# Performance work log

Measured on AMD Instinct MI355X. Metric: run time of the kernel, lower is better.

Reference implementation:

```python
import jax, jax.numpy as jnp
import numpy as np

N = 2048        # num nodes
E = 65536       # num edges
C_IN = 128      # in_channels
C = 128         # out_channels (must equal C_IN for stacked layers)
H = 8           # heads
WALK_LEN = 4
NEG_SLOPE = 0.2


def compute_mask(edge_index, n, walk_length):
    # dense adjacency with duplicate-edge summation (matches sparse_coo to_dense) + self loops
    adj = jnp.zeros((n, n), jnp.float32).at[edge_index[0], edge_index[1]].add(1.0)
    adj = adj + jnp.eye(n, dtype=jnp.float32)
    kernel = jnp.eye(n, dtype=jnp.float32)
    result = kernel
    for _ in range(walk_length):
        kernel = kernel @ adj
        result = result + kernel
    # F.normalize(p=2, dim=1)
    norm = jnp.linalg.norm(result, axis=1, keepdims=True)
    return result / jnp.maximum(norm, 1e-12)


def gkat_layer(x, edge_index, mask, lin_w, att):
    n = x.shape[0]
    xh = (x @ lin_w.T).reshape(n, H, C)              # [N,H,C]
    src, dst = edge_index[0], edge_index[1]          # x_j = xh[src], x_i = xh[dst]
    att_i = att[0, :, :C]                            # [H,C]
    att_j = att[0, :, C:]                            # [H,C]
    # cat([x_i,x_j],-1)*att summed == x_i.att_i + x_j.att_j, computed per node then gathered
    s_i = jnp.einsum('nhc,hc->nh', xh, att_i)
    s_j = jnp.einsum('nhc,hc->nh', xh, att_j)
    alpha = s_i[dst] + s_j[src]                      # [E,H]
    alpha = jnp.where(alpha >= 0, alpha, NEG_SLOPE * alpha)
    alpha = alpha * mask[src, dst][:, None]          # graph-kernel mask per edge
    alpha = jax.nn.softmax(alpha, axis=0)            # global softmax over edges (faithful to F.softmax dim=0)
    # dropout: eval mode -> identity
    msg = xh[src] * alpha[:, :, None]                # [E,H,C]
    out = jax.ops.segment_sum(msg, dst, num_segments=n)  # scatter-add aggregate
    return out.mean(axis=1)                          # head mean -> [N,C]


def setup_inputs() -> dict:
    key = jax.random.key(0)
    ks = jax.random.split(key, 8)
    x = jax.random.normal(ks[0], (N, C_IN), jnp.float32)
    edge_index = jax.random.randint(ks[1], (2, E), 0, N, jnp.int64)
    # xavier-uniform-ish init
    def xav(k, shape):
        fan_in, fan_out = shape[-1], shape[0] if len(shape) == 2 else shape[-1]
        lim = float(np.sqrt(6.0 / (fan_in + fan_out)))
        return jax.random.uniform(k, shape, jnp.float32, -lim, lim)
    lin_w0 = xav(ks[2], (H * C, C_IN))
    att0 = xav(ks[3], (1, H, 2 * C))
    lin_w1 = xav(ks[4], (H * C, C))
    att1 = xav(ks[5], (1, H, 2 * C))
    skip_w = xav(ks[6], (C, C_IN))
    skip_b = jnp.zeros((C,), jnp.float32)
    return {"x": x, "edge_index": edge_index, "lin_w0": lin_w0, "att0": att0,
            "lin_w1": lin_w1, "att1": att1, "skip_w": skip_w, "skip_b": skip_b}


def reference(x, edge_index, lin_w0, att0, lin_w1, att1, skip_w, skip_b):
    mask = compute_mask(edge_index, x.shape[0], WALK_LEN)  # identical for both layers
    x_skip = x @ skip_w.T + skip_b
    h = jax.nn.relu(gkat_layer(x, edge_index, mask, lin_w0, att0))
    h = jax.nn.relu(gkat_layer(h, edge_index, mask, lin_w1, att1))
    return h + x_skip
```

## Files before the change

### kernel.cpp

```cpp
#include <hip/hip_runtime.h>
#include <hip/hip_bf16.h>

#define NN 2048
#define EE 65536
#define HH 8
#define CC 128
#define HC 1024
#define NEG_SLOPE 0.2f

__device__ __forceinline__ unsigned fenc(float f) {
    unsigned u = __float_as_uint(f);
    return (u & 0x80000000u) ? ~u : (u | 0x80000000u);
}
__device__ __forceinline__ float fdec(unsigned e) {
    return (e & 0x80000000u) ? __uint_as_float(e ^ 0x80000000u) : __uint_as_float(~e);
}

__global__ void k_deg(const int* __restrict__ ei, int* __restrict__ deg) {
    int e = blockIdx.x * 256 + threadIdx.x;
    atomicAdd(&deg[ei[EE + e]], 1);
}

__global__ void k_scan(const int* __restrict__ deg, int* __restrict__ offs) {
    __shared__ int buf[2][NN];
    int t = threadIdx.x;
    for (int i = t; i < NN; i += 1024) buf[0][i] = deg[i];
    __syncthreads();
    int cur = 0;
    for (int off = 1; off < NN; off <<= 1) {
        for (int i = t; i < NN; i += 1024) {
            int v = buf[cur][i];
            if (i >= off) v += buf[cur][i - off];
            buf[cur ^ 1][i] = v;
        }
        __syncthreads();
        cur ^= 1;
    }
    if (t == 0) offs[0] = 0;
    for (int i = t; i < NN; i += 1024) offs[i + 1] = buf[cur][i];
}

__global__ void k_scatter(const int* __restrict__ ei, const int* __restrict__ offs,
                          int* __restrict__ cursor, int* __restrict__ elist) {
    int e = blockIdx.x * 256 + threadIdx.x;
    int d = ei[EE + e];
    int p = atomicAdd(&cursor[d], 1);
    elist[offs[d] + p] = e;
}

__global__ __launch_bounds__(256) void k_build_M(
    const int* __restrict__ offs, const int* __restrict__ elist,
    const int* __restrict__ ei, unsigned short* __restrict__ M) {
    int d = blockIdx.x, t = threadIdx.x;
    __shared__ float col[NN];
    __shared__ int s_b[256], s_l[256];
    for (int i = t; i < NN; i += 256) col[i] = 0.f;
    int beg = offs[d], end = offs[d + 1];
    for (int base = beg; base < end; base += 256) {
        int m = min(256, end - base);
        __syncthreads();
        if (t < m) {
            int s = ei[elist[base + t]];
            int b = offs[s];
            s_b[t] = b;
            s_l[t] = offs[s + 1] - b;
            atomicAdd(&col[s], 3.0f);
        }
        __syncthreads();
        for (int i = 0; i < m; i++) {
            int b = s_b[i], l = s_l[i];
            for (int j = t; j < l; j += 256) {
                int u = ei[elist[b + j]];
                atomicAdd(&col[u], 1.0f);
            }
        }
    }
    __syncthreads();
    if (t == 0) col[d] += 3.0f;
    __syncthreads();
    for (int i = t; i < NN; i += 256) M[(size_t)d * NN + i] = (unsigned short)col[i];
}

template <int EDGE_ADD, int DIAG_ADD>
__global__ __launch_bounds__(256) void k_gather(
    const unsigned short* __restrict__ Kin, unsigned short* __restrict__ Kout,
    const int* __restrict__ offs, const int* __restrict__ elist,
    const int* __restrict__ ei) {
    int d = blockIdx.x, t = threadIdx.x;
    int row0 = blockIdx.y * 256;
    __shared__ int ssrc[256];
    __shared__ float extra[256];
    if (EDGE_ADD) extra[t] = 0.f;
    const unsigned short* Kr = Kin + row0 + t;
    float acc = (float)Kr[(size_t)d * NN];
    int beg = offs[d], end = offs[d + 1];
    for (int base = beg; base < end; base += 256) {
        int m = min(256, end - base);
        __syncthreads();
        if (t < m) {
            int s = ei[elist[base + t]];
            ssrc[t] = s;
            if (EDGE_ADD) {
                int ls = s - row0;
                if (ls >= 0 && ls < 256) atomicAdd(&extra[ls], (float)EDGE_ADD);
            }
        }
        __syncthreads();
        int k = 0;
        for (; k + 4 <= m; k += 4) {
            float v0 = (float)Kr[(size_t)ssrc[k + 0] * NN];
            float v1 = (float)Kr[(size_t)ssrc[k + 1] * NN];
            float v2 = (float)Kr[(size_t)ssrc[k + 2] * NN];
            float v3 = (float)Kr[(size_t)ssrc[k + 3] * NN];
            acc += v0 + v1 + v2 + v3;
        }
        for (; k < m; k++) acc += (float)Kr[(size_t)ssrc[k] * NN];
    }
    if (DIAG_ADD && (d - row0) == t) acc += (float)DIAG_ADD;
    if (EDGE_ADD) {
        __syncthreads();
        acc += extra[t];
    }
    Kout[(size_t)d * NN + row0 + t] = (unsigned short)acc;
}

__global__ void k_norm2(const unsigned short* __restrict__ R, float* __restrict__ norm2) {
    int i = blockIdx.x * 256 + threadIdx.x;
    int j0 = blockIdx.y * 128;
    float s = 0.f;
    for (int j = j0; j < j0 + 128; j++) {
        float v = (float)R[(size_t)j * NN + i];
        s += v * v;
    }
    atomicAdd(&norm2[i], s);
}

__global__ void k_mask(const int* __restrict__ ei, const unsigned short* __restrict__ R,
                       const float* __restrict__ norm2, float* __restrict__ mask_e) {
    int e = blockIdx.x * 256 + threadIdx.x;
    int s = ei[e], d = ei[EE + e];
    float r = (float)R[(size_t)d * NN + s];
    float nrm = sqrtf(norm2[s]);
    mask_e[e] = r / fmaxf(nrm, 1e-12f);
}

__global__ __launch_bounds__(256) void gemm_nt(
    const float* __restrict__ A, const float* __restrict__ B,
    const float* __restrict__ bias, float* __restrict__ Cout, int Ncols) {
    __shared__ float As[64][132];
    __shared__ float Bt[128][68];
    int m0 = blockIdx.x * 64, n0 = blockIdx.y * 64;
    int t = threadIdx.x;
    for (int i = t; i < 64 * 32; i += 256) {
        int r = i >> 5, c4 = i & 31;
        float4 v = *(const float4*)(A + (size_t)(m0 + r) * 128 + c4 * 4);
        *(float4*)&As[r][c4 * 4] = v;
    }
    for (int i = t; i < 64 * 32; i += 256) {
        int r = i >> 5, c4 = i & 31;
        float4 v = *(const float4*)(B + (size_t)(n0 + r) * 128 + c4 * 4);
        Bt[c4 * 4 + 0][r] = v.x;
        Bt[c4 * 4 + 1][r] = v.y;
        Bt[c4 * 4 + 2][r] = v.z;
        Bt[c4 * 4 + 3][r] = v.w;
    }
    __syncthreads();
    int ty = t >> 4, tx = t & 15;
    float acc[4][4] = {};
    for (int k = 0; k < 128; k += 4) {
        float4 b0 = *(const float4*)&Bt[k + 0][tx * 4];
        float4 b1 = *(const float4*)&Bt[k + 1][tx * 4];
        float4 b2 = *(const float4*)&Bt[k + 2][tx * 4];
        float4 b3 = *(const float4*)&Bt[k + 3][tx * 4];
#pragma unroll
        for (int r = 0; r < 4; r++) {
            float4 a = *(const float4*)&As[ty * 4 + r][k];
            acc[r][0] += a.x * b0.x + a.y * b1.x + a.z * b2.x + a.w * b3.x;
            acc[r][1] += a.x * b0.y + a.y * b1.y + a.z * b2.y + a.w * b3.y;
            acc[r][2] += a.x * b0.z + a.y * b1.z + a.z * b2.z + a.w * b3.z;
            acc[r][3] += a.x * b0.w + a.y * b1.w + a.z * b2.w + a.w * b3.w;
        }
    }
#pragma unroll
    for (int r = 0; r < 4; r++) {
        int col = n0 + tx * 4;
        float4 o = make_float4(acc[r][0], acc[r][1], acc[r][2], acc[r][3]);
        if (bias) {
            o.x += bias[col + 0]; o.y += bias[col + 1];
            o.z += bias[col + 2]; o.w += bias[col + 3];
        }
        *(float4*)(Cout + (size_t)(m0 + ty * 4 + r) * Ncols + col) = o;
    }
}

__global__ void k_scores(const float* __restrict__ xh, const float* __restrict__ att,
                         float* __restrict__ s_i, float* __restrict__ s_j) {
    int n = blockIdx.x, t = threadIdx.x;
    int h = t >> 5, lane = t & 31;
    const float* xr = xh + (size_t)n * HC + h * CC;
    const float* at = att + h * 2 * CC;
    float ai = 0.f, aj = 0.f;
    for (int c = lane; c < CC; c += 32) {
        float xv = xr[c];
        ai += xv * at[c];
        aj += xv * at[CC + c];
    }
#pragma unroll
    for (int o = 16; o > 0; o >>= 1) {
        ai += __shfl_xor(ai, o);
        aj += __shfl_xor(aj, o);
    }
    if (lane == 0) {
        s_i[n * HH + h] = ai;
        s_j[n * HH + h] = aj;
    }
}

__global__ __launch_bounds__(256) void k_alpha_z(
    const int* __restrict__ ei, const float* __restrict__ s_i,
    const float* __restrict__ s_j, const float* __restrict__ mask_e,
    float* __restrict__ zbuf, unsigned* __restrict__ gmax) {
    int t = threadIdx.x;
    int e = blockIdx.x * 256 + t;
    int s = ei[e], d = ei[EE + e];
    float me = mask_e[e];
    float4 di0 = *(const float4*)(s_i + d * HH);
    float4 di1 = *(const float4*)(s_i + d * HH + 4);
    float4 sj0 = *(const float4*)(s_j + s * HH);
    float4 sj1 = *(const float4*)(s_j + s * HH + 4);
    float z[8] = {di0.x + sj0.x, di0.y + sj0.y, di0.z + sj0.z, di0.w + sj0.w,
                  di1.x + sj1.x, di1.y + sj1.y, di1.z + sj1.z, di1.w + sj1.w};
    __shared__ float smax[HH][256];
#pragma unroll
    for (int h = 0; h < 8; h++) {
        float v = z[h];
        v = (v >= 0.f) ? v : NEG_SLOPE * v;
        v *= me;
        zbuf[(size_t)h * EE + e] = v;
        smax[h][t] = v;
    }
    __syncthreads();
    for (int s2 = 128; s2 > 0; s2 >>= 1) {
        if (t < s2) {
#pragma unroll
            for (int h = 0; h < 8; h++)
                smax[h][t] = fmaxf(smax[h][t], smax[h][t + s2]);
        }
        __syncthreads();
    }
    if (t < 8) atomicMax(&gmax[t], fenc(smax[t][0]));
}

__global__ __launch_bounds__(256) void k_softmax_sum(
    const float* __restrict__ zbuf, const unsigned* __restrict__ gmax,
    float* __restrict__ gsum) {
    int h = blockIdx.y, t = threadIdx.x;
    float mx = fdec(gmax[h]);
    const float* z = zbuf + (size_t)h * EE + blockIdx.x * 2048;
    float s = 0.f;
#pragma unroll
    for (int i = 0; i < 8; i++) s += expf(z[t + i * 256] - mx);
    __shared__ float red[256];
    red[t] = s; __syncthreads();
    for (int s2 = 128; s2 > 0; s2 >>= 1) {
        if (t < s2) red[t] += red[t + s2];
        __syncthreads();
    }
    if (t == 0) atomicAdd(&gsum[h], red[0]);
}

__global__ __launch_bounds__(256) void k_aggregate(
    const float* __restrict__ xh, const float* __restrict__ zbuf,
    const unsigned* __restrict__ gmax, const float* __restrict__ gsum,
    const int* __restrict__ offs, const int* __restrict__ elist,
    const int* __restrict__ ei, const float* __restrict__ skip,
    float* __restrict__ outp, int final_layer) {
    int d = blockIdx.x, t = threadIdx.x;
    int hh = t >> 7, c = t & 127;
    __shared__ float sw[32][8];
    __shared__ int ssrc[32];
    __shared__ float combine[128];
    __shared__ float shh[8], srcp[8];
    if (t < 8) { shh[t] = fdec(gmax[t]); srcp[t] = 1.0f / gsum[t]; }
    float acc = 0.f;
    int beg = offs[d], end = offs[d + 1];
    for (int base = beg; base < end; base += 32) {
        int m = min(32, end - base);
        __syncthreads();
        if (t < m) ssrc[t] = ei[elist[base + t]];
        if (t < m * 8) {
            int k = t >> 3, h = t & 7;
            int e = elist[base + k];
            float z = zbuf[(size_t)h * EE + e];
            sw[k][h] = expf(z - shh[h]) * srcp[h];
        }
        __syncthreads();
        int k = 0;
        for (; k + 2 <= m; k += 2) {
            const float* x0 = xh + (size_t)ssrc[k] * HC + c;
            const float* x1 = xh + (size_t)ssrc[k + 1] * HC + c;
            float a0 = x0[hh * 128], a1 = x0[(hh + 2) * 128];
            float a2 = x0[(hh + 4) * 128], a3 = x0[(hh + 6) * 128];
            float b0 = x1[hh * 128], b1 = x1[(hh + 2) * 128];
            float b2 = x1[(hh + 4) * 128], b3 = x1[(hh + 6) * 128];
            acc += a0 * sw[k][hh] + a1 * sw[k][hh + 2] +
                   a2 * sw[k][hh + 4] + a3 * sw[k][hh + 6] +
                   b0 * sw[k + 1][hh] + b1 * sw[k + 1][hh + 2] +
                   b2 * sw[k + 1][hh + 4] + b3 * sw[k + 1][hh + 6];
        }
        if (k < m) {
            const float* x0 = xh + (size_t)ssrc[k] * HC + c;
            acc += x0[hh * 128] * sw[k][hh] + x0[(hh + 2) * 128] * sw[k][hh + 2] +
                   x0[(hh + 4) * 128] * sw[k][hh + 4] + x0[(hh + 6) * 128] * sw[k][hh + 6];
        }
    }
    if (hh == 0) combine[c] = acc;
    __syncthreads();
    if (hh == 1) combine[c] += acc;
    __syncthreads();
    if (hh == 0) {
        float v = fmaxf(combine[c] * 0.125f, 0.f);
        if (final_layer) v += skip[(size_t)d * CC + c];
        outp[(size_t)d * CC + c] = v;
    }
}

extern "C" void kernel_launch(void* const* d_in, const int* in_sizes, int n_in,
                              void* d_out, int out_size, void* d_ws, size_t ws_size,
                              hipStream_t stream) {
    const float* x    = (const float*)d_in[0];
    const int*   ei   = (const int*)d_in[1];
    const float* w0   = (const float*)d_in[2];
    const float* att0 = (const float*)d_in[3];
    const float* w1   = (const float*)d_in[4];
    const float* att1 = (const float*)d_in[5];
    const float* skw  = (const float*)d_in[6];
    const float* skb  = (const float*)d_in[7];
    float* outp = (float*)d_out;

    char* p = (char*)d_ws;
    auto alloc = [&](size_t bytes) {
        char* r = p;
        p += (bytes + 255) & ~(size_t)255;
        return r;
    };
    unsigned short* Ka = (unsigned short*)alloc((size_t)NN * NN * 2);
    unsigned short* Kb = (unsigned short*)alloc((size_t)NN * NN * 2);
    float* xh     = (float*)alloc((size_t)NN * HC * 4);
    float* h1     = (float*)alloc((size_t)NN * CC * 4);
    float* xskip  = (float*)alloc((size_t)NN * CC * 4);
    float* zbuf   = (float*)alloc((size_t)HH * EE * 4);
    float* mask_e = (float*)alloc((size_t)EE * 4);
    float* s_i    = (float*)alloc((size_t)NN * HH * 4);
    float* s_j    = (float*)alloc((size_t)NN * HH * 4);
    float* norm2  = (float*)alloc((size_t)NN * 4);
    unsigned* gmax = (unsigned*)alloc(HH * 4);
    float* gsum   = (float*)alloc(HH * 4);
    int* deg    = (int*)alloc((size_t)NN * 4);
    int* cursor = (int*)alloc((size_t)NN * 4);
    int* offs   = (int*)alloc((size_t)(NN + 1) * 4);
    int* elist  = (int*)alloc((size_t)EE * 4);

    hipMemsetAsync(deg, 0, (size_t)2 * NN * 4, stream);
    hipMemsetAsync(norm2, 0, (size_t)NN * 4, stream);

    k_deg<<<EE / 256, 256, 0, stream>>>(ei, deg);
    k_scan<<<1, 1024, 0, stream>>>(deg, offs);
    k_scatter<<<EE / 256, 256, 0, stream>>>(ei, offs, cursor, elist);

    k_build_M<<<NN, 256, 0, stream>>>(offs, elist, ei, Ka);
    k_gather<0, 0><<<dim3(NN, 8), 256, 0, stream>>>(Ka, Kb, offs, elist, ei);
    k_gather<1, 2><<<dim3(NN, 8), 256, 0, stream>>>(Kb, Ka, offs, elist, ei);
    k_norm2<<<dim3(NN / 256, 16), 256, 0, stream>>>(Ka, norm2);
    k_mask<<<EE / 256, 256, 0, stream>>>(ei, Ka, norm2, mask_e);

    gemm_nt<<<dim3(32, 2), 256, 0, stream>>>(x, skw, skb, xskip, 128);

    gemm_nt<<<dim3(32, 16), 256, 0, stream>>>(x, w0, nullptr, xh, 1024);
    k_scores<<<NN, 256, 0, stream>>>(xh, att0, s_i, s_j);
    hipMemsetAsync(gmax, 0, 512, stream);
    k_alpha_z<<<EE / 256, 256, 0, stream>>>(ei, s_i, s_j, mask_e, zbuf, gmax);
    k_softmax_sum<<<dim3(32, HH), 256, 0, stream>>>(zbuf, gmax, gsum);
    k_aggregate<<<NN, 256, 0, stream>>>(xh, zbuf, gmax, gsum, offs, elist, ei, nullptr, h1, 0);

    gemm_nt<<<dim3(32, 16), 256, 0, stream>>>(h1, w1, nullptr, xh, 1024);
    k_scores<<<NN, 256, 0, stream>>>(xh, att1, s_i, s_j);
    hipMemsetAsync(gmax, 0, 512, stream);
    k_alpha_z<<<EE / 256, 256, 0, stream>>>(ei, s_i, s_j, mask_e, zbuf, gmax);
    k_softmax_sum<<<dim3(32, HH), 256, 0, stream>>>(zbuf, gmax, gsum);
    k_aggregate<<<NN, 256, 0, stream>>>(xh, zbuf, gmax, gsum, offs, elist, ei, xskip, outp, 1);
}
```

Before: 349.0 us.

## Fuse softmax max and sum passes with a score upper bound; fold norm into gather

The global softmax max is replaced by a per-head upper bound built from the maxima of s_i and s_j, clamped at zero and collected in k_scores. This lets one kernel compute the exp weights and their sums directly, so k_softmax_sum disappears and k_aggregate no longer recomputes exps. The walk-kernel gather now handles two columns per thread with ushort2 loads and half as many blocks. The final gather also accumulates squared row norms, which removes the separate k_norm2 pass. The trade-off is that a loose bound could cause exp underflow, and the norm2 accumulation now issues many more global atomics.

```diff
diff --git a/kernel.cpp b/kernel.cpp
--- a/kernel.cpp
+++ b/kernel.cpp
@@ -81,18 +81,19 @@
     for (int i = t; i < NN; i += 256) M[(size_t)d * NN + i] = (unsigned short)col[i];
 }
 
-template <int EDGE_ADD, int DIAG_ADD>
+template <int EDGE_ADD, int DIAG_ADD, int NORM>
 __global__ __launch_bounds__(256) void k_gather(
     const unsigned short* __restrict__ Kin, unsigned short* __restrict__ Kout,
     const int* __restrict__ offs, const int* __restrict__ elist,
-    const int* __restrict__ ei) {
+    const int* __restrict__ ei, float* __restrict__ norm2) {
     int d = blockIdx.x, t = threadIdx.x;
-    int row0 = blockIdx.y * 256;
+    int row0 = blockIdx.y * 512;
     __shared__ int ssrc[256];
-    __shared__ float extra[256];
-    if (EDGE_ADD) extra[t] = 0.f;
-    const unsigned short* Kr = Kin + row0 + t;
-    float acc = (float)Kr[(size_t)d * NN];
+    __shared__ float extra[512];
+    if (EDGE_ADD) { extra[t] = 0.f; extra[t + 256] = 0.f; }
+    const unsigned short* Kr = Kin + row0 + 2 * t;
+    ushort2 iv = *(const ushort2*)(Kr + (size_t)d * NN);
+    float acc0 = (float)iv.x, acc1 = (float)iv.y;
     int beg = offs[d], end = offs[d + 1];
     for (int base = beg; base < end; base += 256) {
         int m = min(256, end - base);
@@ -102,37 +103,41 @@
             ssrc[t] = s;
             if (EDGE_ADD) {
                 int ls = s - row0;
-                if (ls >= 0 && ls < 256) atomicAdd(&extra[ls], (float)EDGE_ADD);
+                if (ls >= 0 && ls < 512) atomicAdd(&extra[ls], (float)EDGE_ADD);
             }
         }
         __syncthreads();
         int k = 0;
         for (; k + 4 <= m; k += 4) {
-            float v0 = (float)Kr[(size_t)ssrc[k + 0] * NN];
-            float v1 = (float)Kr[(size_t)ssrc[k + 1] * NN];
-            float v2 = (float)Kr[(size_t)ssrc[k + 2] * NN];
-            float v3 = (float)Kr[(size_t)ssrc[k + 3] * NN];
-            acc += v0 + v1 + v2 + v3;
-        }
-        for (; k < m; k++) acc += (float)Kr[(size_t)ssrc[k] * NN];
-    }
-    if (DIAG_ADD && (d - row0) == t) acc += (float)DIAG_ADD;
+            ushort2 v0 = *(const ushort2*)(Kr + (size_t)ssrc[k + 0] * NN);
+            ushort2 v1 = *(const ushort2*)(Kr + (size_t)ssrc[k + 1] * NN);
+            ushort2 v2 = *(const ushort2*)(Kr + (size_t)ssrc[k + 2] * NN);
+            ushort2 v3 = *(const ushort2*)(Kr + (size_t)ssrc[k + 3] * NN);
+            acc0 += (float)(v0.x + v1.x + v2.x + v3.x);
+            acc1 += (float)(v0.y + v1.y + v2.y + v3.y);
+        }
+        for (; k < m; k++) {
+            ushort2 v = *(const ushort2*)(Kr + (size_t)ssrc[k] * NN);
+            acc0 += (float)v.x;
+            acc1 += (float)v.y;
+        }
+    }
+    if (DIAG_ADD) {
+        int dl = d - row0;
+        if (dl == 2 * t) acc0 += (float)DIAG_ADD;
+        if (dl == 2 * t + 1) acc1 += (float)DIAG_ADD;
+    }
     if (EDGE_ADD) {
         __syncthreads();
-        acc += extra[t];
-    }
-    Kout[(size_t)d * NN + row0 + t] = (unsigned short)acc;
-}
-
-__global__ void k_norm2(const unsigned short* __restrict__ R, float* __restrict__ norm2) {
-    int i = blockIdx.x * 256 + threadIdx.x;
-    int j0 = blockIdx.y * 128;
-    float s = 0.f;
-    for (int j = j0; j < j0 + 128; j++) {
-        float v = (float)R[(size_t)j * NN + i];
-        s += v * v;
-    }
-    atomicAdd(&norm2[i], s);
+        acc0 += extra[2 * t];
+        acc1 += extra[2 * t + 1];
+    }
+    *(ushort2*)(Kout + (size_t)d * NN + row0 + 2 * t) =
+        make_ushort2((unsigned short)acc0, (unsigned short)acc1);
+    if (NORM) {
+        atomicAdd(&norm2[row0 + 2 * t], acc0 * acc0);
+        atomicAdd(&norm2[row0 + 2 * t + 1], acc1 * acc1);
+    }
 }
 
 __global__ void k_mask(const int* __restrict__ ei, const unsigned short* __restrict__ R,
@@ -194,7 +199,8 @@
 }
 
 __global__ void k_scores(const float* __restrict__ xh, const float* __restrict__ att,
-                         float* __restrict__ s_i, float* __restrict__ s_j) {
+                         float* __restrict__ s_i, float* __restrict__ s_j,
+                         unsigned* __restrict__ mstat) {
     int n = blockIdx.x, t = threadIdx.x;
     int h = t >> 5, lane = t & 31;
     const float* xr = xh + (size_t)n * HC + h * CC;
@@ -213,15 +219,22 @@
     if (lane == 0) {
         s_i[n * HH + h] = ai;
         s_j[n * HH + h] = aj;
-    }
-}
-
-__global__ __launch_bounds__(256) void k_alpha_z(
+        atomicMax(&mstat[h], fenc(ai));
+        atomicMax(&mstat[HH + h], fenc(aj));
+    }
+}
+
+__global__ __launch_bounds__(256) void k_alpha_sum(
     const int* __restrict__ ei, const float* __restrict__ s_i,
     const float* __restrict__ s_j, const float* __restrict__ mask_e,
-    float* __restrict__ zbuf, unsigned* __restrict__ gmax) {
+    const unsigned* __restrict__ mstat, float* __restrict__ wbuf,
+    float* __restrict__ gsum) {
     int t = threadIdx.x;
     int e = blockIdx.x * 256 + t;
+    __shared__ float Ms[HH];
+    __shared__ float red[HH][256];
+    if (t < HH) Ms[t] = fmaxf(0.f, fdec(mstat[t]) + fdec(mstat[HH + t]));
+    __syncthreads();
     int s = ei[e], d = ei[EE + e];
     float me = mask_e[e];
     float4 di0 = *(const float4*)(s_i + d * HH);
@@ -230,58 +243,38 @@
     float4 sj1 = *(const float4*)(s_j + s * HH + 4);
     float z[8] = {di0.x + sj0.x, di0.y + sj0.y, di0.z + sj0.z, di0.w + sj0.w,
                   di1.x + sj1.x, di1.y + sj1.y, di1.z + sj1.z, di1.w + sj1.w};
-    __shared__ float smax[HH][256];
 #pragma unroll
     for (int h = 0; h < 8; h++) {
         float v = z[h];
         v = (v >= 0.f) ? v : NEG_SLOPE * v;
-        v *= me;
-        zbuf[(size_t)h * EE + e] = v;
-        smax[h][t] = v;
+        float w = expf(v * me - Ms[h]);
+        wbuf[(size_t)h * EE + e] = w;
+        red[h][t] = w;
     }
     __syncthreads();
     for (int s2 = 128; s2 > 0; s2 >>= 1) {
         if (t < s2) {
 #pragma unroll
             for (int h = 0; h < 8; h++)
-                smax[h][t] = fmaxf(smax[h][t], smax[h][t + s2]);
-        }
-        __syncthreads();
-    }
-    if (t < 8) atomicMax(&gmax[t], fenc(smax[t][0]));
-}
-
-__global__ __launch_bounds__(256) void k_softmax_sum(
-    const float* __restrict__ zbuf, const unsigned* __restrict__ gmax,
-    float* __restrict__ gsum) {
-    int h = blockIdx.y, t = threadIdx.x;
-    float mx = fdec(gmax[h]);
-    const float* z = zbuf + (size_t)h * EE + blockIdx.x * 2048;
-    float s = 0.f;
-#pragma unroll
-    for (int i = 0; i < 8; i++) s += expf(z[t + i * 256] - mx);
-    __shared__ float red[256];
-    red[t] = s; __syncthreads();
-    for (int s2 = 128; s2 > 0; s2 >>= 1) {
-        if (t < s2) red[t] += red[t + s2];
-        __syncthreads();
-    }
-    if (t == 0) atomicAdd(&gsum[h], red[0]);
+                red[h][t] += red[h][t + s2];
+        }
+        __syncthreads();
+    }
+    if (t < 8) atomicAdd(&gsum[t], red[t][0]);
 }
 
 __global__ __launch_bounds__(256) void k_aggregate(
-    const float* __restrict__ xh, const float* __restrict__ zbuf,
-    const unsigned* __restrict__ gmax, const float* __restrict__ gsum,
-    const int* __restrict__ offs, const int* __restrict__ elist,
-    const int* __restrict__ ei, const float* __restrict__ skip,
-    float* __restrict__ outp, int final_layer) {
+    const float* __restrict__ xh, const float* __restrict__ wbuf,
+    const float* __restrict__ gsum, const int* __restrict__ offs,
+    const int* __restrict__ elist, const int* __restrict__ ei,
+    const float* __restrict__ skip, float* __restrict__ outp, int final_layer) {
     int d = blockIdx.x, t = threadIdx.x;
     int hh = t >> 7, c = t & 127;
     __shared__ float sw[32][8];
     __shared__ int ssrc[32];
     __shared__ float combine[128];
-    __shared__ float shh[8], srcp[8];
-    if (t < 8) { shh[t] = fdec(gmax[t]); srcp[t] = 1.0f / gsum[t]; }
+    __shared__ float srcp[8];
+    if (t < 8) srcp[t] = 1.0f / gsum[t];
     float acc = 0.f;
     int beg = offs[d], end = offs[d + 1];
     for (int base = beg; base < end; base += 32) {
@@ -290,9 +283,7 @@
         if (t < m) ssrc[t] = ei[elist[base + t]];
         if (t < m * 8) {
             int k = t >> 3, h = t & 7;
-            int e = elist[base + k];
-            float z = zbuf[(size_t)h * EE + e];
-            sw[k][h] = expf(z - shh[h]) * srcp[h];
+            sw[k][h] = wbuf[(size_t)h * EE + elist[base + k]] * srcp[h];
         }
         __syncthreads();
         int k = 0;
@@ -349,12 +340,12 @@
     float* xh     = (float*)alloc((size_t)NN * HC * 4);
     float* h1     = (float*)alloc((size_t)NN * CC * 4);
     float* xskip  = (float*)alloc((size_t)NN * CC * 4);
-    float* zbuf   = (float*)alloc((size_t)HH * EE * 4);
+    float* wbuf   = (float*)alloc((size_t)HH * EE * 4);
     float* mask_e = (float*)alloc((size_t)EE * 4);
     float* s_i    = (float*)alloc((size_t)NN * HH * 4);
     float* s_j    = (float*)alloc((size_t)NN * HH * 4);
     float* norm2  = (float*)alloc((size_t)NN * 4);
-    unsigned* gmax = (unsigned*)alloc(HH * 4);
+    unsigned* mstat = (unsigned*)alloc(16 * 4);
     float* gsum   = (float*)alloc(HH * 4);
     int* deg    = (int*)alloc((size_t)NN * 4);
     int* cursor = (int*)alloc((size_t)NN * 4);
@@ -369,24 +360,21 @@
     k_scatter<<<EE / 256, 256, 0, stream>>>(ei, offs, cursor, elist);
 
     k_build_M<<<NN, 256, 0, stream>>>(offs, elist, ei, Ka);
-    k_gather<0, 0><<<dim3(NN, 8), 256, 0, stream>>>(Ka, Kb, offs, elist, ei);
-    k_gather<1, 2><<<dim3(NN, 8), 256, 0, stream>>>(Kb, Ka, offs, elist, ei);
-    k_norm2<<<dim3(NN / 256, 16), 256, 0, stream>>>(Ka, norm2);
+    k_gather<0, 0, 0><<<dim3(NN, 4), 256, 0, stream>>>(Ka, Kb, offs, elist, ei, norm2);
+    k_gather<1, 2, 1><<<dim3(NN, 4), 256, 0, stream>>>(Kb, Ka, offs, elist, ei, norm2);
     k_mask<<<EE / 256, 256, 0, stream>>>(ei, Ka, norm2, mask_e);
 
     gemm_nt<<<dim3(32, 2), 256, 0, stream>>>(x, skw, skb, xskip, 128);
 
     gemm_nt<<<dim3(32, 16), 256, 0, stream>>>(x, w0, nullptr, xh, 1024);
-    k_scores<<<NN, 256, 0, stream>>>(xh, att0, s_i, s_j);
-    hipMemsetAsync(gmax, 0, 512, stream);
-    k_alpha_z<<<EE / 256, 256, 0, stream>>>(ei, s_i, s_j, mask_e, zbuf, gmax);
-    k_softmax_sum<<<dim3(32, HH), 256, 0, stream>>>(zbuf, gmax, gsum);
-    k_aggregate<<<NN, 256, 0, stream>>>(xh, zbuf, gmax, gsum, offs, elist, ei, nullptr, h1, 0);
+    hipMemsetAsync(mstat, 0, 512, stream);
+    k_scores<<<NN, 256, 0, stream>>>(xh, att0, s_i, s_j, mstat);
+    k_alpha_sum<<<EE / 256, 256, 0, stream>>>(ei, s_i, s_j, mask_e, mstat, wbuf, gsum);
+    k_aggregate<<<NN, 256, 0, stream>>>(xh, wbuf, gsum, offs, elist, ei, nullptr, h1, 0);
 
     gemm_nt<<<dim3(32, 16), 256, 0, stream>>>(h1, w1, nullptr, xh, 1024);
-    k_scores<<<NN, 256, 0, stream>>>(xh, att1, s_i, s_j);
-    hipMemsetAsync(gmax, 0, 512, stream);
-    k_alpha_z<<<EE / 256, 256, 0, stream>>>(ei, s_i, s_j, mask_e, zbuf, gmax);
-    k_softmax_sum<<<dim3(32, HH), 256, 0, stream>>>(zbuf, gmax, gsum);
-    k_aggregate<<<NN, 256, 0, stream>>>(xh, zbuf, gmax, gsum, offs, elist, ei, xskip, outp, 1);
-}
+    hipMemsetAsync(mstat, 0, 512, stream);
+    k_scores<<<NN, 256, 0, stream>>>(xh, att1, s_i, s_j, mstat);
+    k_alpha_sum<<<EE / 256, 256, 0, stream>>>(ei, s_i, s_j, mask_e, mstat, wbuf, gsum);
+    k_aggregate<<<NN, 256, 0, stream>>>(xh, wbuf, gsum, offs, elist, ei, xskip, outp, 1);
+}
```

Result: slower. 884.0 us (+153.3%).
